# Optimization experiments

Measured on AMD Instinct MI355X. Metric: run time of the kernel, lower is better.

## Reference

```python
import jax, jax.numpy as jnp
import numpy as np


def gcn_conv(h, W, b, src, dst):
    # PyG GCNConv: h @ W, add self-loops, symmetric deg^-1/2 normalization,
    # scatter-add messages from src to dst, then add bias.
    n = h.shape[0]
    h = h @ W                                   # [N, out]
    loop = jnp.arange(n, dtype=src.dtype)
    row = jnp.concatenate([src, loop])          # message sources
    col = jnp.concatenate([dst, loop])          # aggregation targets
    deg = jax.ops.segment_sum(jnp.ones_like(col, dtype=h.dtype), col, num_segments=n)
    dinv = jnp.where(deg > 0, jax.lax.rsqrt(deg), 0.0)
    norm = dinv[row] * dinv[col]                # [E+N]
    out = jax.ops.segment_sum(h[row] * norm[:, None], col, num_segments=n)
    return out + b


def setup_inputs() -> dict:
    key = jax.random.key(0)
    ks = jax.random.split(key, 12)
    N, E = 50000, 800000
    in_dim, hid, out_dim = 768, 256, 128
    x = jax.random.normal(ks[0], (N, in_dim), dtype=jnp.float32)
    edge_index = jax.random.randint(ks[1], (2, E), 0, N, dtype=jnp.int64)

    def lin(k, fan_in, fan_out):
        bound = 1.0 / np.sqrt(fan_in)
        kw, kb = jax.random.split(k)
        W = jax.random.uniform(kw, (fan_in, fan_out), jnp.float32, -bound, bound)
        b = jax.random.uniform(kb, (fan_out,), jnp.float32, -bound, bound)
        return W, b

    W1, b1 = lin(ks[2], in_dim, hid)
    Wg1, bg1 = lin(ks[3], hid, hid)
    Wg2, bg2 = lin(ks[4], hid, hid)
    W2, b2 = lin(ks[5], hid, out_dim)
    Wc, bc = lin(ks[6], out_dim, 2)
    return {
        "x": x, "edge_index": edge_index,
        "W1": W1, "b1": b1, "Wg1": Wg1, "bg1": bg1,
        "Wg2": Wg2, "bg2": bg2, "W2": W2, "b2": b2,
        "Wc": Wc, "bc": bc, "batch_size": 1024,
    }


def reference(x, edge_index, W1, b1, Wg1, bg1, Wg2, bg2, W2, b2, Wc, bc, batch_size):
    src, dst = edge_index[0], edge_index[1]
    h = jax.nn.relu(x @ W1 + b1)                # linear_relu1
    h = gcn_conv(h, Wg1, bg1, src, dst)         # text1
    # dropout is identity in eval mode
    h = gcn_conv(h, Wg2, bg2, src, dst)         # text2
    h = jax.nn.relu(h @ W2 + b2)                # linear_relu2
    logits = h @ Wc + bc                        # classifier
    return logits[:batch_size]
```

## Files before the change

kernel.cpp:

```cpp
#include <hip/hip_runtime.h>
#include <hip/hip_bf16.h>
#include <cstdint>
#include <cstddef>
#include <type_traits>

typedef _Float16 half8 __attribute__((ext_vector_type(8)));
typedef _Float16 half4v __attribute__((ext_vector_type(4)));
typedef float float4v __attribute__((ext_vector_type(4)));


__global__ void k_prep(int* __restrict__ cnt, int* __restrict__ flag,
                       const float* __restrict__ W1, const float* __restrict__ Wg1,
                       const float* __restrict__ Wg2, _Float16* __restrict__ W1t,
                       _Float16* __restrict__ Wg1t, _Float16* __restrict__ Wg2t,
                       int n, int in_dim, int hid) {
  int idx = blockIdx.x * blockDim.x + threadIdx.x;
  if (idx < n) { cnt[idx] = 0; flag[idx] = 0; return; }
  int w = idx - n;
  int n1 = in_dim * hid;
  int n2 = hid * hid;
  if (w < n1) {
    int nn = w / in_dim, k = w - nn * in_dim;
    W1t[w] = (_Float16)W1[(size_t)k * hid + nn];
  } else if (w < n1 + n2) {
    int i2 = w - n1;
    int nn = i2 / hid, k = i2 - nn * hid;
    Wg1t[i2] = (_Float16)Wg1[(size_t)k * hid + nn];
  } else if (w < n1 + 2 * n2) {
    int i2 = w - n1 - n2;
    int nn = i2 / hid, k = i2 - nn * hid;
    Wg2t[i2] = (_Float16)Wg2[(size_t)k * hid + nn];
  }
}


__global__ void k_countmark(const int* __restrict__ src, const int* __restrict__ dst,
                            int* __restrict__ cnt, int* __restrict__ flag,
                            int E, int Batch) {
  int e = blockIdx.x * blockDim.x + threadIdx.x;
  if (e < E) {
    int d = dst[e];
    atomicAdd(&cnt[d], 1);
    if (d < Batch) flag[src[e]] = 1;
  }
  if (e < Batch) flag[e] = 1;
}


__global__ __launch_bounds__(1024) void k_scan_local_dual(const int* __restrict__ cnt,
                                                          const int* __restrict__ flag,
                                                          int* __restrict__ rowp,
                                                          int* __restrict__ fidx,
                                                          int* __restrict__ bsumc,
                                                          int* __restrict__ bsumf, int n) {
  __shared__ int smc[1024];
  __shared__ int smf[1024];
  int tid = threadIdx.x;
  int i = blockIdx.x * 1024 + tid;
  int vc = (i < n) ? cnt[i] : 0;
  int vf = (i < n) ? flag[i] : 0;
  smc[tid] = vc;
  smf[tid] = vf;
  __syncthreads();
  for (int off = 1; off < 1024; off <<= 1) {
    int tc_ = (tid >= off) ? smc[tid - off] : 0;
    int tf_ = (tid >= off) ? smf[tid - off] : 0;
    __syncthreads();
    smc[tid] += tc_;
    smf[tid] += tf_;
    __syncthreads();
  }
  if (i < n) {
    rowp[i] = smc[tid] - vc;
    fidx[i] = smf[tid] - vf;
  }
  if (tid == 1023) { bsumc[blockIdx.x] = smc[1023]; bsumf[blockIdx.x] = smf[1023]; }
}

__global__ __launch_bounds__(1024) void k_scan_sums_dual(int* __restrict__ bsumc,
                                                         int* __restrict__ bsumf, int nb) {
  __shared__ int smc[1024];
  __shared__ int smf[1024];
  int tid = threadIdx.x;
  int vc = (tid < nb) ? bsumc[tid] : 0;
  int vf = (tid < nb) ? bsumf[tid] : 0;
  smc[tid] = vc;
  smf[tid] = vf;
  __syncthreads();
  for (int off = 1; off < 1024; off <<= 1) {
    int tc_ = (tid >= off) ? smc[tid - off] : 0;
    int tf_ = (tid >= off) ? smf[tid - off] : 0;
    __syncthreads();
    smc[tid] += tc_;
    smf[tid] += tf_;
    __syncthreads();
  }
  if (tid < nb) { bsumc[tid] = smc[tid] - vc; bsumf[tid] = smf[tid] - vf; }
}

__global__ void k_finalize_all(int* __restrict__ rowp, int* __restrict__ fidx,
                               const int* __restrict__ bsumc, const int* __restrict__ bsumf,
                               const int* __restrict__ cnt, const int* __restrict__ flag,
                               int* __restrict__ cursor, float* __restrict__ dinv,
                               int* __restrict__ list, int* __restrict__ s1cnt,
                               int n, int E) {
  int i = blockIdx.x * blockDim.x + threadIdx.x;
  if (i < n) {
    int v = rowp[i] + bsumc[i >> 10];
    rowp[i] = v;
    cursor[i] = v;
    dinv[i] = rsqrtf((float)(cnt[i] + 1));
    int f = flag[i];
    int fp = fidx[i] + bsumf[i >> 10];
    if (f) list[fp] = i;
    if (i == n - 1) { s1cnt[0] = fp + f; rowp[n] = E; }
  }
}

__global__ void k_fill(const int* __restrict__ src, const int* __restrict__ dst,
                       int* __restrict__ cursor, int* __restrict__ csr_src, int E) {
  int e = blockIdx.x * blockDim.x + threadIdx.x;
  if (e < E) {
    int pos = atomicAdd(&cursor[dst[e]], 1);
    csr_src[pos] = src[e];
  }
}


__device__ __forceinline__ void gl_lds16(const void* g, void* l) {
  __builtin_amdgcn_global_load_lds(
      (const __attribute__((address_space(1))) void*)g,
      (__attribute__((address_space(3))) void*)l, 16, 0, 0);
}

#define VMCNT(n) asm volatile("s_waitcnt vmcnt(" #n ")" ::: "memory")

template <int RA>
__device__ __forceinline__ void dma_tile(const char* const (&aS)[RA], const int (&aD)[RA],
                                         const char* const (&bS)[2], const int (&bD)[2],
                                         char* ab, char* bb, size_t advA, size_t advB) {
#pragma unroll
  for (int rr = 0; rr < RA; ++rr) gl_lds16(aS[rr] + advA, ab + aD[rr]);
#pragma unroll
  for (int rr = 0; rr < 2; ++rr) gl_lds16(bS[rr] + advB, bb + bD[rr]);
}

template <typename AT, int RELU, int BIAS, int SCALE, int GATHER>
__global__ __launch_bounds__(512) void k_gemm_mfma(const AT* __restrict__ A,
                                                   const _Float16* __restrict__ Bt,
                                                   const float* __restrict__ bias,
                                                   const float* __restrict__ rowscale,
                                                   _Float16* __restrict__ out,
                                                   int M, int N, int K,
                                                   const int* __restrict__ ridx,
                                                   const int* __restrict__ rcnt) {
  __shared__ alignas(16) AT Asm[2][128 * 32];
  __shared__ alignas(16) _Float16 Bsm[2][256 * 32];
  constexpr bool AF32 = std::is_same_v<AT, float>;
  constexpr int RA = AF32 ? 2 : 1;
  constexpr int ABUFB = 128 * 32 * (int)sizeof(AT);
  constexpr int BBUFB = 256 * 32 * 2;

  const int tid = threadIdx.x;
  const int wv = tid >> 6;
  const int ln = tid & 63;
  const int quad = ln >> 4;
  const int l15 = ln & 15;
  const int wm = (wv >> 2) * 64;
  const int wn = (wv & 3) * 64;

  const int bm = (int)blockIdx.x * 128;

  int Meff = M;
  if constexpr (GATHER) {
    Meff = rcnt[0];
    if (bm >= Meff) return;
  }

  const char* aSrcB[RA];
  int aDstOff[RA];
#pragma unroll
  for (int rr = 0; rr < RA; ++rr) {
    int q = rr * 8192 + wv * 1024 + ln * 16;
    int row, colE;
    if constexpr (AF32) {
      int h = q >> 13;
      int q13 = q & 8191;
      row = q13 >> 6;
      colE = ((q13 & 63) >> 2) + (h << 4);
    } else {
      row = q >> 6;
      colE = (q & 63) >> 1;
    }
    int li = bm + row; if (li > Meff - 1) li = Meff - 1;
    int grow;
    if constexpr (GATHER) grow = ridx[li]; else grow = li;
    aSrcB[rr] = (const char*)(A + (size_t)grow * K + colE);
    aDstOff[rr] = rr * 8192 + wv * 1024;
  }
  const char* bSrcB[2];
  int bDstOff[2];
#pragma unroll
  for (int rr = 0; rr < 2; ++rr) {
    int q = rr * 8192 + wv * 1024 + ln * 16;
    int row = q >> 6;
    int colH = (q & 63) >> 1;
    bSrcB[rr] = (const char*)(Bt + (size_t)row * K + colH);
    bDstOff[rr] = rr * 8192 + wv * 1024;
  }

  float4v acc[4][4];
#pragma unroll
  for (int i = 0; i < 4; ++i)
#pragma unroll
    for (int j = 0; j < 4; ++j) acc[i][j] = (float4v){0.f, 0.f, 0.f, 0.f};

  const int nk = K >> 5;

  char* const Ab0 = (char*)&Asm[0][0];
  char* const Bb0 = (char*)&Bsm[0][0];

  dma_tile<RA>(aSrcB, aDstOff, bSrcB, bDstOff, Ab0, Bb0, 0, 0);
  dma_tile<RA>(aSrcB, aDstOff, bSrcB, bDstOff, Ab0 + ABUFB, Bb0 + BBUFB,
               (size_t)32 * sizeof(AT), 64);

  int buf = 0;
  for (int kt = 0; kt < nk; ++kt) {
    if (kt + 1 < nk) {
      if constexpr (AF32) { VMCNT(4); } else { VMCNT(3); }
    } else {
      VMCNT(0);
    }
    __builtin_amdgcn_sched_barrier(0);
    __builtin_amdgcn_s_barrier();
    __builtin_amdgcn_sched_barrier(0);

    const AT* Ab = &Asm[buf][0];
    const _Float16* Bb = &Bsm[buf][0];
    half8 bf[4];
#pragma unroll
    for (int j = 0; j < 4; ++j)
      bf[j] = *(const half8*)(Bb + (wn + j * 16 + l15) * 32 + quad * 8);
#pragma unroll
    for (int i = 0; i < 4; ++i) {
      int rowa = wm + i * 16 + l15;
      half8 af;
      if constexpr (AF32) {
        const float* ap = Ab + (quad >> 1) * 2048 + rowa * 16 + (quad & 1) * 8;
        float4v f0 = *(const float4v*)ap;
        float4v f1 = *(const float4v*)(ap + 4);
        af[0] = (_Float16)f0[0]; af[1] = (_Float16)f0[1];
        af[2] = (_Float16)f0[2]; af[3] = (_Float16)f0[3];
        af[4] = (_Float16)f1[0]; af[5] = (_Float16)f1[1];
        af[6] = (_Float16)f1[2]; af[7] = (_Float16)f1[3];
      } else {
        af = *(const half8*)(Ab + rowa * 32 + quad * 8);
      }
#pragma unroll
      for (int j = 0; j < 4; ++j)
        acc[i][j] = __builtin_amdgcn_mfma_f32_16x16x32_f16(af, bf[j], acc[i][j], 0, 0, 0);
    }

    __builtin_amdgcn_s_barrier();
    __builtin_amdgcn_sched_barrier(0);

    if (kt + 2 < nk) {
      dma_tile<RA>(aSrcB, aDstOff, bSrcB, bDstOff,
                   Ab0 + (size_t)buf * ABUFB, Bb0 + (size_t)buf * BBUFB,
                   (size_t)(kt + 2) * 32 * sizeof(AT), (size_t)(kt + 2) * 64);
      __builtin_amdgcn_sched_barrier(0);
    }

    buf ^= 1;
  }

#pragma unroll
  for (int j = 0; j < 4; ++j) {
    int c = wn + j * 16 + l15;
    float bv = BIAS ? bias[c] : 0.f;
#pragma unroll
    for (int i = 0; i < 4; ++i) {
      int rbase = bm + wm + i * 16 + quad * 4;
      float4v a = acc[i][j];
#pragma unroll
      for (int reg = 0; reg < 4; ++reg) {
        int r = rbase + reg;
        if (r < Meff) {
          int orow;
          if constexpr (GATHER) orow = ridx[r]; else orow = r;
          float v = a[reg] + bv;
          if (RELU) v = fmaxf(v, 0.f);
          if (SCALE) v *= rowscale[orow];
          out[(size_t)orow * N + c] = (_Float16)v;
        }
      }
    }
  }
}


template <typename OT>
__global__ __launch_bounds__(256) void k_agg(const _Float16* __restrict__ t,
                                             const int* __restrict__ row_ptr,
                                             const int* __restrict__ csr_src,
                                             const float* __restrict__ dinv,
                                             const float* __restrict__ bias,
                                             OT* __restrict__ out, int n_nodes) {
  int w = (int)((blockIdx.x * 256 + threadIdx.x) >> 6);
  int lane = threadIdx.x & 63;
  if (w >= n_nodes) return;
  float di = dinv[w];
  half4v v = *(const half4v*)(t + (size_t)w * 256 + lane * 4);
  float ax = (float)v[0], ay = (float)v[1], az = (float)v[2], aw = (float)v[3];
  int e0 = row_ptr[w], e1 = row_ptr[w + 1];
  int e = e0;
  for (; e + 4 <= e1; e += 4) {
    int s0 = csr_src[e];
    int s1 = csr_src[e + 1];
    int s2 = csr_src[e + 2];
    int s3 = csr_src[e + 3];
    half4v u0 = *(const half4v*)(t + (size_t)s0 * 256 + lane * 4);
    half4v u1 = *(const half4v*)(t + (size_t)s1 * 256 + lane * 4);
    half4v u2 = *(const half4v*)(t + (size_t)s2 * 256 + lane * 4);
    half4v u3 = *(const half4v*)(t + (size_t)s3 * 256 + lane * 4);
    ax += (float)u0[0] + (float)u1[0] + (float)u2[0] + (float)u3[0];
    ay += (float)u0[1] + (float)u1[1] + (float)u2[1] + (float)u3[1];
    az += (float)u0[2] + (float)u1[2] + (float)u2[2] + (float)u3[2];
    aw += (float)u0[3] + (float)u1[3] + (float)u2[3] + (float)u3[3];
  }
  for (; e < e1; ++e) {
    int s = csr_src[e];
    half4v u = *(const half4v*)(t + (size_t)s * 256 + lane * 4);
    ax += (float)u[0]; ay += (float)u[1]; az += (float)u[2]; aw += (float)u[3];
  }
  const float4 b = ((const float4*)bias)[lane];
  if constexpr (std::is_same_v<OT, float>) {
    float4 o;
    o.x = ax * di + b.x; o.y = ay * di + b.y;
    o.z = az * di + b.z; o.w = aw * di + b.w;
    ((float4*)(out + (size_t)w * 256))[lane] = o;
  } else {
    half4v o;
    o[0] = (_Float16)(ax * di + b.x); o[1] = (_Float16)(ay * di + b.y);
    o[2] = (_Float16)(az * di + b.z); o[3] = (_Float16)(aw * di + b.w);
    *(half4v*)(out + (size_t)w * 256 + lane * 4) = o;
  }
}

__global__ __launch_bounds__(256) void k_agg_g(const _Float16* __restrict__ t,
                                               const int* __restrict__ row_ptr,
                                               const int* __restrict__ csr_src,
                                               const float* __restrict__ dinv,
                                               const float* __restrict__ bias,
                                               _Float16* __restrict__ out,
                                               const int* __restrict__ list,
                                               const int* __restrict__ s1cnt) {
  int wi = (int)((blockIdx.x * 256 + threadIdx.x) >> 6);
  int lane = threadIdx.x & 63;
  if (wi >= s1cnt[0]) return;
  int w = list[wi];
  float di = dinv[w];
  half4v v = *(const half4v*)(t + (size_t)w * 256 + lane * 4);
  float ax = (float)v[0], ay = (float)v[1], az = (float)v[2], aw = (float)v[3];
  int e0 = row_ptr[w], e1 = row_ptr[w + 1];
  int e = e0;
  for (; e + 4 <= e1; e += 4) {
    int s0 = csr_src[e];
    int s1 = csr_src[e + 1];
    int s2 = csr_src[e + 2];
    int s3 = csr_src[e + 3];
    half4v u0 = *(const half4v*)(t + (size_t)s0 * 256 + lane * 4);
    half4v u1 = *(const half4v*)(t + (size_t)s1 * 256 + lane * 4);
    half4v u2 = *(const half4v*)(t + (size_t)s2 * 256 + lane * 4);
    half4v u3 = *(const half4v*)(t + (size_t)s3 * 256 + lane * 4);
    ax += (float)u0[0] + (float)u1[0] + (float)u2[0] + (float)u3[0];
    ay += (float)u0[1] + (float)u1[1] + (float)u2[1] + (float)u3[1];
    az += (float)u0[2] + (float)u1[2] + (float)u2[2] + (float)u3[2];
    aw += (float)u0[3] + (float)u1[3] + (float)u2[3] + (float)u3[3];
  }
  for (; e < e1; ++e) {
    int s = csr_src[e];
    half4v u = *(const half4v*)(t + (size_t)s * 256 + lane * 4);
    ax += (float)u[0]; ay += (float)u[1]; az += (float)u[2]; aw += (float)u[3];
  }
  const float4 b = ((const float4*)bias)[lane];
  half4v o;
  o[0] = (_Float16)(ax * di + b.x); o[1] = (_Float16)(ay * di + b.y);
  o[2] = (_Float16)(az * di + b.z); o[3] = (_Float16)(aw * di + b.w);
  *(half4v*)(out + (size_t)w * 256 + lane * 4) = o;
}


__global__ __launch_bounds__(256) void k_tail(const float* __restrict__ A,
                                              const float* __restrict__ B,
                                              const float* __restrict__ b2,
                                              const float* __restrict__ Wc,
                                              const float* __restrict__ bc,
                                              float* __restrict__ out,
                                              int M, int N, int K) {
  __shared__ float As[16][68];
  __shared__ float Bs[16][136];
  __shared__ float wsm[256];
  __shared__ float red[64][16][2];
  const int bm = blockIdx.x * 64;
  const int tid = threadIdx.x;
  const int tr = (tid >> 4) << 2;
  const int tc = (tid & 15) << 3;
  const int lm  = tid >> 2;
  const int lk  = (tid & 3) << 2;
  const int lk2 = tid >> 4;
  const int ln  = (tid & 15) << 3;
  wsm[tid] = Wc[tid];
  const bool arow_ok = (bm + lm) < M;
  const float* Aptr = A + (size_t)(bm + lm) * K + lk;
  const float* Bptr = B + (size_t)lk2 * N + ln;
  float acc[4][8] = {};
  for (int k0 = 0; k0 < K; k0 += 16) {
    float4 a4 = make_float4(0.f, 0.f, 0.f, 0.f);
    if (arow_ok) a4 = *(const float4*)(Aptr + k0);
    float4 b4 = *(const float4*)(Bptr + (size_t)k0 * N);
    float4 b5 = *(const float4*)(Bptr + (size_t)k0 * N + 4);
    As[lk + 0][lm] = a4.x;
    As[lk + 1][lm] = a4.y;
    As[lk + 2][lm] = a4.z;
    As[lk + 3][lm] = a4.w;
    *(float4*)&Bs[lk2][ln] = b4;
    *(float4*)&Bs[lk2][ln + 4] = b5;
    __syncthreads();
#pragma unroll
    for (int k = 0; k < 16; ++k) {
      float4 av = *(const float4*)&As[k][tr];
      float a[4] = {av.x, av.y, av.z, av.w};
      float b[8];
      *(float4*)&b[0] = *(const float4*)&Bs[k][tc];
      *(float4*)&b[4] = *(const float4*)&Bs[k][tc + 4];
#pragma unroll
      for (int i = 0; i < 4; ++i)
#pragma unroll
        for (int j = 0; j < 8; ++j) acc[i][j] += a[i] * b[j];
    }
    __syncthreads();
  }
  float p[4][2] = {};
#pragma unroll
  for (int j = 0; j < 8; ++j) {
    float bb = b2[tc + j];
    float w0 = wsm[(tc + j) * 2 + 0];
    float w1 = wsm[(tc + j) * 2 + 1];
#pragma unroll
    for (int i = 0; i < 4; ++i) {
      float v = fmaxf(acc[i][j] + bb, 0.f);
      p[i][0] += v * w0;
      p[i][1] += v * w1;
    }
  }
#pragma unroll
  for (int i = 0; i < 4; ++i) {
    red[tr + i][tid & 15][0] = p[i][0];
    red[tr + i][tid & 15][1] = p[i][1];
  }
  __syncthreads();
  if (tid < 128) {
    int row = tid >> 1, kk = tid & 1;
    float s = 0.f;
#pragma unroll
    for (int t = 0; t < 16; ++t) s += red[row][t][kk];
    int r = bm + row;
    if (r < M) out[2 * r + kk] = s + bc[kk];
  }
}


extern "C" void kernel_launch(void* const* d_in, const int* in_sizes, int n_in,
                              void* d_out, int out_size, void* d_ws, size_t ws_size,
                              hipStream_t stream) {
  const float* x   = (const float*)d_in[0];
  const int*   ei  = (const int*)d_in[1];
  const float* W1  = (const float*)d_in[2];
  const float* b1  = (const float*)d_in[3];
  const float* Wg1 = (const float*)d_in[4];
  const float* bg1 = (const float*)d_in[5];
  const float* Wg2 = (const float*)d_in[6];
  const float* bg2 = (const float*)d_in[7];
  const float* W2  = (const float*)d_in[8];
  const float* b2  = (const float*)d_in[9];
  const float* Wc  = (const float*)d_in[10];
  const float* bc  = (const float*)d_in[11];
  float* out = (float*)d_out;

  const int hid     = in_sizes[3];
  const int in_dim  = in_sizes[2] / hid;
  const int out_dim = in_sizes[9];
  const int N       = in_sizes[0] / in_dim;
  const int E       = in_sizes[1] / 2;
  const int Batch   = out_size / 2;

  const int* srcI = ei;
  const int* dstI = ei + E;

  char* ws = (char*)d_ws;
  size_t off = 0;
  auto alloc = [&](size_t bytes) -> void* {
    void* p = ws + off;
    off = (off + bytes + 255) & ~(size_t)255;
    return p;
  };
  _Float16* h0h  = (_Float16*)alloc((size_t)N * hid * 2);
  _Float16* t1h  = (_Float16*)alloc((size_t)N * hid * 2);
  _Float16* h1h  = (_Float16*)alloc((size_t)N * hid * 2);
  _Float16* t2h  = (_Float16*)alloc((size_t)N * hid * 2);
  _Float16* W1t  = (_Float16*)alloc((size_t)in_dim * hid * 2);
  _Float16* Wg1t = (_Float16*)alloc((size_t)hid * hid * 2);
  _Float16* Wg2t = (_Float16*)alloc((size_t)hid * hid * 2);
  float* agg2    = (float*)alloc((size_t)Batch * hid * 4);
  float* dinv    = (float*)alloc((size_t)N * 4);
  int*   cnt     = (int*)alloc((size_t)N * 4);
  int*   rowp    = (int*)alloc((size_t)(N + 1) * 4);
  int*   fidx    = (int*)alloc((size_t)N * 4);
  int*   bsumc   = (int*)alloc((size_t)1024 * 4);
  int*   bsumf   = (int*)alloc((size_t)1024 * 4);
  int*   cursor  = (int*)alloc((size_t)N * 4);
  int*   csrs    = (int*)alloc((size_t)E * 4);
  int*   flag    = (int*)alloc((size_t)N * 4);
  int*   list    = (int*)alloc((size_t)N * 4);
  int*   s1cnt   = (int*)alloc((size_t)64);
  (void)ws_size; (void)n_in;

  dim3 blk(256);
  const int nb = (N + 1023) / 1024;

  {
    int total = N + in_dim * hid + 2 * hid * hid;
    k_prep<<<(total + 255) / 256, blk, 0, stream>>>(cnt, flag, W1, Wg1, Wg2,
                                                    W1t, Wg1t, Wg2t, N, in_dim, hid);
  }
  k_countmark<<<(E + 255) / 256, blk, 0, stream>>>(srcI, dstI, cnt, flag, E, Batch);
  k_scan_local_dual<<<nb, 1024, 0, stream>>>(cnt, flag, rowp, fidx, bsumc, bsumf, N);
  k_scan_sums_dual<<<1, 1024, 0, stream>>>(bsumc, bsumf, nb);
  k_finalize_all<<<(N + 255) / 256, blk, 0, stream>>>(rowp, fidx, bsumc, bsumf, cnt, flag,
                                                      cursor, dinv, list, s1cnt, N, E);
  k_fill<<<(E + 255) / 256, blk, 0, stream>>>(srcI, dstI, cursor, csrs, E);

  const int ng = (N + 127) / 128;
  dim3 gblk(512);
  k_gemm_mfma<float, 1, 1, 0, 0><<<dim3(ng), gblk, 0, stream>>>(x, W1t, b1, nullptr, h0h, N, hid, in_dim, nullptr, nullptr);
  k_gemm_mfma<_Float16, 0, 0, 1, 0><<<dim3(ng), gblk, 0, stream>>>(h0h, Wg1t, nullptr, dinv, t1h, N, hid, hid, nullptr, nullptr);
  k_agg_g<<<(N + 3) / 4, blk, 0, stream>>>(t1h, rowp, csrs, dinv, bg1, h1h, list, s1cnt);
  k_gemm_mfma<_Float16, 0, 0, 1, 1><<<dim3(ng), gblk, 0, stream>>>(h1h, Wg2t, nullptr, dinv, t2h, N, hid, hid, list, s1cnt);
  k_agg<float><<<(Batch + 3) / 4, blk, 0, stream>>>(t2h, rowp, csrs, dinv, bg2, agg2, Batch);
  k_tail<<<(Batch + 63) / 64, blk, 0, stream>>>(agg2, W2, b2, Wc, bc, out, Batch, out_dim, hid);
}
```

Baseline: 484.1 us.

## Replace LDS-staged MFMA GEMM with register-direct loads and 64-row tiles

The GEMM kernel no longer stages tiles through shared memory with global_load_lds DMA and barriers. Each wave now loads its A and B fragments straight from global memory into registers, double-buffered by hand across k-steps, with 256-thread blocks covering 64 rows by 256 columns. This removes LDS traffic and block-wide barriers. In exchange, all four waves in a block reload the same A rows from global memory, and fragment loads are narrow strided row reads, so the kernel leans on cache and gives up shared-memory reuse.

```diff
diff --git a/kernel.cpp b/kernel.cpp
--- a/kernel.cpp
+++ b/kernel.cpp
@@ -127,49 +127,55 @@
 }
 
 
-__device__ __forceinline__ void gl_lds16(const void* g, void* l) {
-  __builtin_amdgcn_global_load_lds(
-      (const __attribute__((address_space(1))) void*)g,
-      (__attribute__((address_space(3))) void*)l, 16, 0, 0);
-}
-
-#define VMCNT(n) asm volatile("s_waitcnt vmcnt(" #n ")" ::: "memory")
-
-template <int RA>
-__device__ __forceinline__ void dma_tile(const char* const (&aS)[RA], const int (&aD)[RA],
-                                         const char* const (&bS)[2], const int (&bD)[2],
-                                         char* ab, char* bb, size_t advA, size_t advB) {
-#pragma unroll
-  for (int rr = 0; rr < RA; ++rr) gl_lds16(aS[rr] + advA, ab + aD[rr]);
-#pragma unroll
-  for (int rr = 0; rr < 2; ++rr) gl_lds16(bS[rr] + advB, bb + bD[rr]);
+template <typename AT>
+__device__ __forceinline__ void load_a4(const AT* const (&ap)[4], int k0, half8 (&d)[4]) {
+#pragma unroll
+  for (int i = 0; i < 4; ++i) {
+    if constexpr (std::is_same_v<AT, float>) {
+      float4v f0 = *(const float4v*)(ap[i] + k0);
+      float4v f1 = *(const float4v*)(ap[i] + k0 + 4);
+      half8 h;
+      h[0] = (_Float16)f0[0]; h[1] = (_Float16)f0[1];
+      h[2] = (_Float16)f0[2]; h[3] = (_Float16)f0[3];
+      h[4] = (_Float16)f1[0]; h[5] = (_Float16)f1[1];
+      h[6] = (_Float16)f1[2]; h[7] = (_Float16)f1[3];
+      d[i] = h;
+    } else {
+      d[i] = *(const half8*)(ap[i] + k0);
+    }
+  }
+}
+
+__device__ __forceinline__ void load_b4(const _Float16* const (&bp)[4], int k0, half8 (&d)[4]) {
+#pragma unroll
+  for (int j = 0; j < 4; ++j) d[j] = *(const half8*)(bp[j] + k0);
+}
+
+__device__ __forceinline__ void mfma16(const half8 (&a)[4], const half8 (&b)[4],
+                                       float4v (&acc)[4][4]) {
+#pragma unroll
+  for (int i = 0; i < 4; ++i)
+#pragma unroll
+    for (int j = 0; j < 4; ++j)
+      acc[i][j] = __builtin_amdgcn_mfma_f32_16x16x32_f16(a[i], b[j], acc[i][j], 0, 0, 0);
 }
 
 template <typename AT, int RELU, int BIAS, int SCALE, int GATHER>
-__global__ __launch_bounds__(512) void k_gemm_mfma(const AT* __restrict__ A,
-                                                   const _Float16* __restrict__ Bt,
-                                                   const float* __restrict__ bias,
-                                                   const float* __restrict__ rowscale,
-                                                   _Float16* __restrict__ out,
-                                                   int M, int N, int K,
-                                                   const int* __restrict__ ridx,
-                                                   const int* __restrict__ rcnt) {
-  __shared__ alignas(16) AT Asm[2][128 * 32];
-  __shared__ alignas(16) _Float16 Bsm[2][256 * 32];
-  constexpr bool AF32 = std::is_same_v<AT, float>;
-  constexpr int RA = AF32 ? 2 : 1;
-  constexpr int ABUFB = 128 * 32 * (int)sizeof(AT);
-  constexpr int BBUFB = 256 * 32 * 2;
-
+__global__ __launch_bounds__(256) void k_gemm_reg(const AT* __restrict__ A,
+                                                  const _Float16* __restrict__ Bt,
+                                                  const float* __restrict__ bias,
+                                                  const float* __restrict__ rowscale,
+                                                  _Float16* __restrict__ out,
+                                                  int M, int N, int K,
+                                                  const int* __restrict__ ridx,
+                                                  const int* __restrict__ rcnt) {
   const int tid = threadIdx.x;
   const int wv = tid >> 6;
   const int ln = tid & 63;
   const int quad = ln >> 4;
   const int l15 = ln & 15;
-  const int wm = (wv >> 2) * 64;
-  const int wn = (wv & 3) * 64;
-
-  const int bm = (int)blockIdx.x * 128;
+  const int wn = wv * 64;
+  const int bm = (int)blockIdx.x * 64;
 
   int Meff = M;
   if constexpr (GATHER) {
@@ -177,37 +183,19 @@
     if (bm >= Meff) return;
   }
 
-  const char* aSrcB[RA];
-  int aDstOff[RA];
-#pragma unroll
-  for (int rr = 0; rr < RA; ++rr) {
-    int q = rr * 8192 + wv * 1024 + ln * 16;
-    int row, colE;
-    if constexpr (AF32) {
-      int h = q >> 13;
-      int q13 = q & 8191;
-      row = q13 >> 6;
-      colE = ((q13 & 63) >> 2) + (h << 4);
-    } else {
-      row = q >> 6;
-      colE = (q & 63) >> 1;
-    }
-    int li = bm + row; if (li > Meff - 1) li = Meff - 1;
+  const AT* ap[4];
+#pragma unroll
+  for (int i = 0; i < 4; ++i) {
+    int li = bm + i * 16 + l15;
+    if (li > Meff - 1) li = Meff - 1;
     int grow;
     if constexpr (GATHER) grow = ridx[li]; else grow = li;
-    aSrcB[rr] = (const char*)(A + (size_t)grow * K + colE);
-    aDstOff[rr] = rr * 8192 + wv * 1024;
-  }
-  const char* bSrcB[2];
-  int bDstOff[2];
-#pragma unroll
-  for (int rr = 0; rr < 2; ++rr) {
-    int q = rr * 8192 + wv * 1024 + ln * 16;
-    int row = q >> 6;
-    int colH = (q & 63) >> 1;
-    bSrcB[rr] = (const char*)(Bt + (size_t)row * K + colH);
-    bDstOff[rr] = rr * 8192 + wv * 1024;
-  }
+    ap[i] = A + (size_t)grow * K + quad * 8;
+  }
+  const _Float16* bp[4];
+#pragma unroll
+  for (int j = 0; j < 4; ++j)
+    bp[j] = Bt + (size_t)(wn + j * 16 + l15) * K + quad * 8;
 
   float4v acc[4][4];
 #pragma unroll
@@ -217,61 +205,18 @@
 
   const int nk = K >> 5;
 
-  char* const Ab0 = (char*)&Asm[0][0];
-  char* const Bb0 = (char*)&Bsm[0][0];
-
-  dma_tile<RA>(aSrcB, aDstOff, bSrcB, bDstOff, Ab0, Bb0, 0, 0);
-  dma_tile<RA>(aSrcB, aDstOff, bSrcB, bDstOff, Ab0 + ABUFB, Bb0 + BBUFB,
-               (size_t)32 * sizeof(AT), 64);
-
-  int buf = 0;
-  for (int kt = 0; kt < nk; ++kt) {
-    if (kt + 1 < nk) {
-      if constexpr (AF32) { VMCNT(4); } else { VMCNT(3); }
-    } else {
-      VMCNT(0);
+  half8 ae[4], ao[4], be[4], bo[4];
+  load_a4<AT>(ap, 0, ae);
+  load_b4(bp, 0, be);
+  for (int kt = 0; kt < nk; kt += 2) {
+    load_a4<AT>(ap, (kt + 1) << 5, ao);
+    load_b4(bp, (kt + 1) << 5, bo);
+    mfma16(ae, be, acc);
+    if (kt + 2 < nk) {
+      load_a4<AT>(ap, (kt + 2) << 5, ae);
+      load_b4(bp, (kt + 2) << 5, be);
     }
-    __builtin_amdgcn_sched_barrier(0);
-    __builtin_amdgcn_s_barrier();
-    __builtin_amdgcn_sched_barrier(0);
-
-    const AT* Ab = &Asm[buf][0];
-    const _Float16* Bb = &Bsm[buf][0];
-    half8 bf[4];
-#pragma unroll
-    for (int j = 0; j < 4; ++j)
-      bf[j] = *(const half8*)(Bb + (wn + j * 16 + l15) * 32 + quad * 8);
-#pragma unroll
-    for (int i = 0; i < 4; ++i) {
-      int rowa = wm + i * 16 + l15;
-      half8 af;
-      if constexpr (AF32) {
-        const float* ap = Ab + (quad >> 1) * 2048 + rowa * 16 + (quad & 1) * 8;
-        float4v f0 = *(const float4v*)ap;
-        float4v f1 = *(const float4v*)(ap + 4);
-        af[0] = (_Float16)f0[0]; af[1] = (_Float16)f0[1];
-        af[2] = (_Float16)f0[2]; af[3] = (_Float16)f0[3];
-        af[4] = (_Float16)f1[0]; af[5] = (_Float16)f1[1];
-        af[6] = (_Float16)f1[2]; af[7] = (_Float16)f1[3];
-      } else {
-        af = *(const half8*)(Ab + rowa * 32 + quad * 8);
-      }
-#pragma unroll
-      for (int j = 0; j < 4; ++j)
-        acc[i][j] = __builtin_amdgcn_mfma_f32_16x16x32_f16(af, bf[j], acc[i][j], 0, 0, 0);
-    }
-
-    __builtin_amdgcn_s_barrier();
-    __builtin_amdgcn_sched_barrier(0);
-
-    if (kt + 2 < nk) {
-      dma_tile<RA>(aSrcB, aDstOff, bSrcB, bDstOff,
-                   Ab0 + (size_t)buf * ABUFB, Bb0 + (size_t)buf * BBUFB,
-                   (size_t)(kt + 2) * 32 * sizeof(AT), (size_t)(kt + 2) * 64);
-      __builtin_amdgcn_sched_barrier(0);
-    }
-
-    buf ^= 1;
+    mfma16(ao, bo, acc);
   }
 
 #pragma unroll
@@ -280,7 +225,7 @@
     float bv = BIAS ? bias[c] : 0.f;
 #pragma unroll
     for (int i = 0; i < 4; ++i) {
-      int rbase = bm + wm + i * 16 + quad * 4;
+      int rbase = bm + i * 16 + quad * 4;
       float4v a = acc[i][j];
 #pragma unroll
       for (int reg = 0; reg < 4; ++reg) {
@@ -541,12 +486,11 @@
                                                       cursor, dinv, list, s1cnt, N, E);
   k_fill<<<(E + 255) / 256, blk, 0, stream>>>(srcI, dstI, cursor, csrs, E);
 
-  const int ng = (N + 127) / 128;
-  dim3 gblk(512);
-  k_gemm_mfma<float, 1, 1, 0, 0><<<dim3(ng), gblk, 0, stream>>>(x, W1t, b1, nullptr, h0h, N, hid, in_dim, nullptr, nullptr);
-  k_gemm_mfma<_Float16, 0, 0, 1, 0><<<dim3(ng), gblk, 0, stream>>>(h0h, Wg1t, nullptr, dinv, t1h, N, hid, hid, nullptr, nullptr);
+  const int ng = (N + 63) / 64;
+  k_gemm_reg<float, 1, 1, 0, 0><<<dim3(ng), blk, 0, stream>>>(x, W1t, b1, nullptr, h0h, N, hid, in_dim, nullptr, nullptr);
+  k_gemm_reg<_Float16, 0, 0, 1, 0><<<dim3(ng), blk, 0, stream>>>(h0h, Wg1t, nullptr, dinv, t1h, N, hid, hid, nullptr, nullptr);
   k_agg_g<<<(N + 3) / 4, blk, 0, stream>>>(t1h, rowp, csrs, dinv, bg1, h1h, list, s1cnt);
-  k_gemm_mfma<_Float16, 0, 0, 1, 1><<<dim3(ng), gblk, 0, stream>>>(h1h, Wg2t, nullptr, dinv, t2h, N, hid, hid, list, s1cnt);
+  k_gemm_reg<_Float16, 0, 0, 1, 1><<<dim3(ng), blk, 0, stream>>>(h1h, Wg2t, nullptr, dinv, t2h, N, hid, hid, list, s1cnt);
   k_agg<float><<<(Batch + 3) / 4, blk, 0, stream>>>(t2h, rowp, csrs, dinv, bg2, agg2, Batch);
   k_tail<<<(Batch + 63) / 64, blk, 0, stream>>>(agg2, W2, b2, Wc, bc, out, Batch, out_dim, hid);
 }
```

Measured after the change: 581.5 us. +20.1%, slower.
